# Kernel tuning notes

Hardware: AMD Instinct MI355X
Metric: run time of the kernel (lower is better)

## Reference

```python
import jax, jax.numpy as jnp
import numpy as np

INPUT_LAYER_SIZE = 40960 * 2
LAYER1_SIZE = 512
LAYER2_SIZE = 32
LAYER3_SIZE = 32
BATCH = 4096


def setup_inputs() -> dict:
    key = jax.random.key(0)
    ks = jax.random.split(key, 10)
    # Sparse one-hot style features: mostly zeros with ~30 active entries per side.
    def sparse_features(k, n_active=30):
        kidx, = jax.random.split(k, 1)
        idx = jax.random.randint(kidx, (BATCH, n_active), 0, 40960)
        feats = jnp.zeros((BATCH, 40960), dtype=jnp.float32)
        return feats.at[jnp.arange(BATCH)[:, None], idx].set(1.0)
    w_features = sparse_features(ks[0])
    b_features = sparse_features(ks[1])
    s_in = 1.0 / np.sqrt(INPUT_LAYER_SIZE)
    s1 = 1.0 / np.sqrt(LAYER1_SIZE)
    s2 = 1.0 / np.sqrt(LAYER2_SIZE)
    s3 = 1.0 / np.sqrt(LAYER3_SIZE)
    return {
        "w_features": w_features,
        "b_features": b_features,
        "W_in": jax.random.uniform(ks[2], (LAYER1_SIZE, INPUT_LAYER_SIZE), jnp.float32, -s_in, s_in),
        "b_in": jax.random.uniform(ks[3], (LAYER1_SIZE,), jnp.float32, -s_in, s_in),
        "W1": jax.random.uniform(ks[4], (LAYER2_SIZE, LAYER1_SIZE), jnp.float32, -s1, s1),
        "b1": jax.random.uniform(ks[5], (LAYER2_SIZE,), jnp.float32, -s1, s1),
        "W2": jax.random.uniform(ks[6], (LAYER3_SIZE, LAYER2_SIZE), jnp.float32, -s2, s2),
        "b2": jax.random.uniform(ks[7], (LAYER3_SIZE,), jnp.float32, -s2, s2),
        "W3": jax.random.uniform(ks[8], (1, LAYER3_SIZE), jnp.float32, -s3, s3),
        "b3": jax.random.uniform(ks[9], (1,), jnp.float32, -s3, s3),
    }


def reference(w_features, b_features, W_in, b_in, W1, b1, W2, b2, W3, b3):
    # Concatenate both perspectives: [B, 81920]
    x = jnp.concatenate([w_features, b_features], axis=1)
    # Huge sparse-input accumulator layer (the kernel-headroom op)
    accum = x @ W_in.T + b_in                       # [B, 512]
    l1 = jnp.clip(accum, 0.0, 1.0)                  # clipped ReLU
    l2 = jnp.clip(l1 @ W1.T + b1, 0.0, 1.0)         # [B, 32]
    l3 = jnp.clip(l2 @ W2.T + b2, 0.0, 1.0)         # [B, 32]
    return l3 @ W3.T + b3                           # [B, 1]
```

## Files before the change

kernel.cpp:

```cpp
#include <hip/hip_runtime.h>
#include <hip/hip_bf16.h>

#define IN_PER_SIDE   40960
#define IN_TOTAL      81920
#define L1            512
#define L2            32
#define L3_           32
#define BATCH         4096
#define MAXIDX        128

typedef float        v4f __attribute__((ext_vector_type(4)));
typedef float        v8f __attribute__((ext_vector_type(8)));
typedef _Float16     v4h __attribute__((ext_vector_type(4)));
typedef _Float16     v8h __attribute__((ext_vector_type(8)));
typedef unsigned int v4u __attribute__((ext_vector_type(4)));

#define WT_BYTES ((size_t)IN_TOTAL * L1 * sizeof(_Float16))

__global__ __launch_bounds__(256) void transpose_win(
    const float* __restrict__ W, _Float16* __restrict__ WTh)
{
    __shared__ float tile[64][65];
    const int jt = blockIdx.x * 64;
    const int ot = blockIdx.y * 64;

    {
        const int tx = threadIdx.x & 15;
        const int ty = threadIdx.x >> 4;
#pragma unroll
        for (int k = 0; k < 4; ++k) {
            const int o = ty + 16 * k;
            const v4f* p = (const v4f*)&W[(size_t)(ot + o) * IN_TOTAL + jt + 4 * tx];
            v4f v = __builtin_nontemporal_load(p);
            tile[4 * tx + 0][o] = v.x;
            tile[4 * tx + 1][o] = v.y;
            tile[4 * tx + 2][o] = v.z;
            tile[4 * tx + 3][o] = v.w;
        }
    }
    __syncthreads();
    {
        const int tx = threadIdx.x & 7;
        const int ty = threadIdx.x >> 3;
#pragma unroll
        for (int k = 0; k < 2; ++k) {
            const int j = ty + 32 * k;
            v8f v;
#pragma unroll
            for (int c = 0; c < 8; ++c) v[c] = tile[j][8 * tx + c];
            v8h h = __builtin_convertvector(v, v8h);
            *(v8h*)&WTh[(size_t)(jt + j) * L1 + ot + 8 * tx] = h;
        }
    }
}

__global__ __launch_bounds__(512) void nnue_fused(
    const float* __restrict__ wf, const float* __restrict__ bfeat,
    const _Float16* __restrict__ WTh,
    const float* __restrict__ b_in,
    const float* __restrict__ W1, const float* __restrict__ b1,
    const float* __restrict__ W2, const float* __restrict__ b2,
    const float* __restrict__ W3, const float* __restrict__ b3,
    float* __restrict__ out)
{
    const int b = blockIdx.x;
    const int t = threadIdx.x;

    __shared__ int   sidx[MAXIDX];
    __shared__ int   scnt;
    __shared__ float accs[8 * 64 * 9];
    __shared__ float l1s[L1];
    __shared__ float l2acc[L2];
    __shared__ float l2s[L2];
    __shared__ float l3s[L3_];

    if (t == 0) { scnt = 0; sidx[0] = 0; }
    __syncthreads();

    const v4u* wrow = (const v4u*)(wf    + (size_t)b * IN_PER_SIDE);
    const v4u* brow = (const v4u*)(bfeat + (size_t)b * IN_PER_SIDE);

    for (int g = 0; g < 5; ++g) {
        v4u a0, a1, a2, a3, c0, c1, c2, c3;
        {
            const int i0 = t + (4 * g + 0) * 512;
            const int i1 = t + (4 * g + 1) * 512;
            const int i2 = t + (4 * g + 2) * 512;
            const int i3 = t + (4 * g + 3) * 512;
            a0 = wrow[i0]; a1 = wrow[i1]; a2 = wrow[i2]; a3 = wrow[i3];
            c0 = brow[i0]; c1 = brow[i1]; c2 = brow[i2]; c3 = brow[i3];
        }
#pragma unroll
        for (int u = 0; u < 4; ++u) {
            const v4u a = (u == 0) ? a0 : (u == 1) ? a1 : (u == 2) ? a2 : a3;
            const v4u c = (u == 0) ? c0 : (u == 1) ? c1 : (u == 2) ? c2 : c3;
            const int i = t + (4 * g + u) * 512;
            if (a.x | a.y | a.z | a.w) {
                if (a.x) sidx[atomicAdd(&scnt, 1)] = 4 * i + 0;
                if (a.y) sidx[atomicAdd(&scnt, 1)] = 4 * i + 1;
                if (a.z) sidx[atomicAdd(&scnt, 1)] = 4 * i + 2;
                if (a.w) sidx[atomicAdd(&scnt, 1)] = 4 * i + 3;
            }
            if (c.x | c.y | c.z | c.w) {
                if (c.x) sidx[atomicAdd(&scnt, 1)] = IN_PER_SIDE + 4 * i + 0;
                if (c.y) sidx[atomicAdd(&scnt, 1)] = IN_PER_SIDE + 4 * i + 1;
                if (c.z) sidx[atomicAdd(&scnt, 1)] = IN_PER_SIDE + 4 * i + 2;
                if (c.w) sidx[atomicAdd(&scnt, 1)] = IN_PER_SIDE + 4 * i + 3;
            }
        }
    }
    __syncthreads();

    const int n = scnt;
    const int w = t >> 6;
    const int l = t & 63;
    const v8h* WTH8 = (const v8h*)WTh;

    v8f acc0 = {0, 0, 0, 0, 0, 0, 0, 0};
    v8f acc1 = {0, 0, 0, 0, 0, 0, 0, 0};
    const int J     = (n + 7) >> 3;
    const int Jeven = (J + 1) & ~1;

    {
        const int f0 = w, f1 = w + 8;
        v8h h0 = WTH8[(size_t)sidx[f0 < n ? f0 : 0] * 64 + l];
        float s0 = (f0 < n) ? 1.0f : 0.0f;
        v8h h1 = WTH8[(size_t)sidx[f1 < n ? f1 : 0] * 64 + l];
        float s1 = (f1 < n) ? 1.0f : 0.0f;
        for (int j = 2; j < Jeven; j += 2) {
            const int g0 = w + 8 * j, g1 = g0 + 8;
            v8h p0 = WTH8[(size_t)sidx[g0 < n ? g0 : 0] * 64 + l];
            const float u0 = (g0 < n) ? 1.0f : 0.0f;
            v8h p1 = WTH8[(size_t)sidx[g1 < n ? g1 : 0] * 64 + l];
            const float u1 = (g1 < n) ? 1.0f : 0.0f;
            acc0 += s0 * __builtin_convertvector(h0, v8f);
            acc1 += s1 * __builtin_convertvector(h1, v8f);
            h0 = p0; s0 = u0; h1 = p1; s1 = u1;
        }
        acc0 += s0 * __builtin_convertvector(h0, v8f);
        acc1 += s1 * __builtin_convertvector(h1, v8f);
    }
    acc0 += acc1;

    {
        float* dst = &accs[(w * 64 + l) * 9];
#pragma unroll
        for (int i = 0; i < 8; ++i) dst[i] = acc0[i];
    }
    __syncthreads();

    {
        const int ll = t >> 3, c = t & 7;
        float s = 0.0f;
#pragma unroll
        for (int ww = 0; ww < 8; ++ww) s += accs[(ww * 64 + ll) * 9 + c];
        l1s[t] = fminf(fmaxf(s + b_in[t], 0.0f), 1.0f);
    }
    __syncthreads();

    {
        const int kk = t >> 4;
        const int gg = t & 15;
        const float* wp = W1 + (size_t)kk * L1;
        float p = 0.0f;
        for (int o = gg; o < L1; o += 16) p += wp[o] * l1s[o];
#pragma unroll
        for (int off = 8; off > 0; off >>= 1) p += __shfl_down(p, off, 16);
        if (gg == 0) l2acc[kk] = p;
    }
    __syncthreads();
    if (t < L2) l2s[t] = fminf(fmaxf(l2acc[t] + b1[t], 0.0f), 1.0f);
    __syncthreads();

    if (t < L3_) {
        const float* wp = W2 + (size_t)t * L2;
        float p = b2[t];
#pragma unroll
        for (int q = 0; q < L2; ++q) p += wp[q] * l2s[q];
        l3s[t] = fminf(fmaxf(p, 0.0f), 1.0f);
    }
    __syncthreads();

    if (t == 0) {
        float p = b3[0];
#pragma unroll
        for (int q = 0; q < L3_; ++q) p += W3[q] * l3s[q];
        out[b] = p;
    }
}

__global__ __launch_bounds__(512) void nnue_fallback(
    const float* __restrict__ wf, const float* __restrict__ bfeat,
    const float* __restrict__ W_in, const float* __restrict__ b_in,
    const float* __restrict__ W1, const float* __restrict__ b1,
    const float* __restrict__ W2, const float* __restrict__ b2,
    const float* __restrict__ W3, const float* __restrict__ b3,
    float* __restrict__ out)
{
    const int b = blockIdx.x;
    const int t = threadIdx.x;
    __shared__ int   idxs[MAXIDX];
    __shared__ int   scnt;
    __shared__ float l1s[L1];
    __shared__ float l2acc[L2];
    __shared__ float l2s[L2];
    __shared__ float l3s[L3_];

    if (t == 0) scnt = 0;
    __syncthreads();
    const v4f* wrow = (const v4f*)(wf    + (size_t)b * IN_PER_SIDE);
    const v4f* brow = (const v4f*)(bfeat + (size_t)b * IN_PER_SIDE);
    for (int i = t; i < IN_PER_SIDE / 4; i += 512) {
        v4f v = wrow[i];
        if (v.x != 0.0f) idxs[atomicAdd(&scnt, 1)] = 4 * i + 0;
        if (v.y != 0.0f) idxs[atomicAdd(&scnt, 1)] = 4 * i + 1;
        if (v.z != 0.0f) idxs[atomicAdd(&scnt, 1)] = 4 * i + 2;
        if (v.w != 0.0f) idxs[atomicAdd(&scnt, 1)] = 4 * i + 3;
        v4f u = brow[i];
        if (u.x != 0.0f) idxs[atomicAdd(&scnt, 1)] = IN_PER_SIDE + 4 * i + 0;
        if (u.y != 0.0f) idxs[atomicAdd(&scnt, 1)] = IN_PER_SIDE + 4 * i + 1;
        if (u.z != 0.0f) idxs[atomicAdd(&scnt, 1)] = IN_PER_SIDE + 4 * i + 2;
        if (u.w != 0.0f) idxs[atomicAdd(&scnt, 1)] = IN_PER_SIDE + 4 * i + 3;
    }
    __syncthreads();
    const int n = scnt;
    float a0 = 0.0f;
    const float* row = W_in + (size_t)t * IN_TOTAL;
    for (int i = 0; i < n; ++i) a0 += row[idxs[i]];
    l1s[t] = fminf(fmaxf(b_in[t] + a0, 0.0f), 1.0f);
    __syncthreads();
    {
        const int k = t >> 4, g = t & 15;
        const float* wp = W1 + (size_t)k * L1;
        float p = 0.0f;
        for (int o = g; o < L1; o += 16) p += wp[o] * l1s[o];
#pragma unroll
        for (int off = 8; off > 0; off >>= 1) p += __shfl_down(p, off, 16);
        if (g == 0) l2acc[k] = p;
    }
    __syncthreads();
    if (t < L2) l2s[t] = fminf(fmaxf(l2acc[t] + b1[t], 0.0f), 1.0f);
    __syncthreads();
    if (t < L3_) {
        const float* wp = W2 + (size_t)t * L2;
        float p = b2[t];
#pragma unroll
        for (int q = 0; q < L2; ++q) p += wp[q] * l2s[q];
        l3s[t] = fminf(fmaxf(p, 0.0f), 1.0f);
    }
    __syncthreads();
    if (t == 0) {
        float p = b3[0];
#pragma unroll
        for (int q = 0; q < L3_; ++q) p += W3[q] * l3s[q];
        out[b] = p;
    }
}

extern "C" void kernel_launch(void* const* d_in, const int* in_sizes, int n_in,
                              void* d_out, int out_size, void* d_ws, size_t ws_size,
                              hipStream_t stream) {
    const float* wf   = (const float*)d_in[0];
    const float* bfeat= (const float*)d_in[1];
    const float* W_in = (const float*)d_in[2];
    const float* b_in = (const float*)d_in[3];
    const float* W1   = (const float*)d_in[4];
    const float* b1   = (const float*)d_in[5];
    const float* W2   = (const float*)d_in[6];
    const float* b2   = (const float*)d_in[7];
    const float* W3   = (const float*)d_in[8];
    const float* b3   = (const float*)d_in[9];
    float* out = (float*)d_out;

    if (ws_size >= WT_BYTES) {
        _Float16* WTh = (_Float16*)d_ws;
        dim3 grid(IN_TOTAL / 64, L1 / 64);
        transpose_win<<<grid, 256, 0, stream>>>(W_in, WTh);
        nnue_fused<<<BATCH, 512, 0, stream>>>(
            wf, bfeat, WTh, b_in, W1, b1, W2, b2, W3, b3, out);
    } else {
        nnue_fallback<<<BATCH, 512, 0, stream>>>(
            wf, bfeat, W_in, b_in, W1, b1, W2, b2, W3, b3, out);
    }
}
```

Before: 1.359 ms.

## Fuse weight transpose and sparse index scan into one cooperative persistent kernel

Adds a persistent cooperative kernel that transposes and converts W_in to fp16 while the same blocks scan the feature rows into a global index list. A grid-wide sync then separates this from the gather/accumulate and MLP stage. The goal is to overlap the feature scan with the weight transpose and to remove a separate launch. The cost is a grid sync, an extra global round trip for the indices, and a cap of 1024 persistent blocks that may reduce parallelism in the gather stage. It falls back to the old two-kernel path if the cooperative launch is unavailable.

After: 1.542 ms. 1.13x slower.

```diff
diff --git a/kernel.cpp b/kernel.cpp
--- a/kernel.cpp
+++ b/kernel.cpp
@@ -1,5 +1,8 @@
 #include <hip/hip_runtime.h>
 #include <hip/hip_bf16.h>
+#include <hip/hip_cooperative_groups.h>
+
+namespace cg = cooperative_groups;
 
 #define IN_PER_SIDE   40960
 #define IN_TOTAL      81920
@@ -16,6 +19,179 @@
 typedef unsigned int v4u __attribute__((ext_vector_type(4)));
 
 #define WT_BYTES ((size_t)IN_TOTAL * L1 * sizeof(_Float16))
+#define CNT_OFF  WT_BYTES
+#define IDX_OFF  (WT_BYTES + 16384)
+#define WS_NEED  (IDX_OFF + (size_t)BATCH * MAXIDX * 4)
+
+__global__ __launch_bounds__(512) void nnue_mega(
+    const float* __restrict__ W, _Float16* __restrict__ WTh,
+    const float* __restrict__ wf, const float* __restrict__ bfeat,
+    int* __restrict__ cnt, int* __restrict__ idxg,
+    const float* __restrict__ b_in,
+    const float* __restrict__ W1, const float* __restrict__ b1,
+    const float* __restrict__ W2, const float* __restrict__ b2,
+    const float* __restrict__ W3, const float* __restrict__ b3,
+    float* __restrict__ out)
+{
+    const int t = threadIdx.x;
+    const int G = gridDim.x;
+
+    __shared__ __align__(16) char smem[8 * 64 * 9 * 4];
+    float (*tile)[65] = reinterpret_cast<float (*)[65]>(smem);
+    float* accs = reinterpret_cast<float*>(smem);
+    __shared__ int   sidx[MAXIDX];
+    __shared__ int   scnt;
+    __shared__ float l1s[L1];
+    __shared__ float l2acc[L2];
+    __shared__ float l2s[L2];
+    __shared__ float l3s[L3_];
+
+    for (int tid = blockIdx.x; tid < 1280 * 8; tid += G) {
+        const int jt = (tid % 1280) * 64;
+        const int ot = (tid / 1280) * 64;
+        {
+            const int tx = t & 15;
+            const int ty = t >> 4;
+#pragma unroll
+            for (int k = 0; k < 2; ++k) {
+                const int o = ty + 32 * k;
+                const v4f* p = (const v4f*)&W[(size_t)(ot + o) * IN_TOTAL + jt + 4 * tx];
+                v4f v = __builtin_nontemporal_load(p);
+                tile[4 * tx + 0][o] = v.x;
+                tile[4 * tx + 1][o] = v.y;
+                tile[4 * tx + 2][o] = v.z;
+                tile[4 * tx + 3][o] = v.w;
+            }
+        }
+        __syncthreads();
+        {
+            const int tx = t & 7;
+            const int ty = t >> 3;
+            v8f v;
+#pragma unroll
+            for (int c = 0; c < 8; ++c) v[c] = tile[ty][8 * tx + c];
+            v8h h = __builtin_convertvector(v, v8h);
+            *(v8h*)&WTh[(size_t)(jt + ty) * L1 + ot + 8 * tx] = h;
+        }
+        __syncthreads();
+    }
+
+    for (int row = blockIdx.x; row < BATCH; row += G) {
+        if (t == 0) scnt = 0;
+        __syncthreads();
+        const v4u* wrow = (const v4u*)(wf    + (size_t)row * IN_PER_SIDE);
+        const v4u* brow = (const v4u*)(bfeat + (size_t)row * IN_PER_SIDE);
+        for (int i = t; i < IN_PER_SIDE / 4; i += 512) {
+            v4u a = __builtin_nontemporal_load(wrow + i);
+            v4u c = __builtin_nontemporal_load(brow + i);
+            if (a.x | a.y | a.z | a.w) {
+                if (a.x) { int p = atomicAdd(&scnt, 1); if (p < MAXIDX) sidx[p] = 4 * i + 0; }
+                if (a.y) { int p = atomicAdd(&scnt, 1); if (p < MAXIDX) sidx[p] = 4 * i + 1; }
+                if (a.z) { int p = atomicAdd(&scnt, 1); if (p < MAXIDX) sidx[p] = 4 * i + 2; }
+                if (a.w) { int p = atomicAdd(&scnt, 1); if (p < MAXIDX) sidx[p] = 4 * i + 3; }
+            }
+            if (c.x | c.y | c.z | c.w) {
+                if (c.x) { int p = atomicAdd(&scnt, 1); if (p < MAXIDX) sidx[p] = IN_PER_SIDE + 4 * i + 0; }
+                if (c.y) { int p = atomicAdd(&scnt, 1); if (p < MAXIDX) sidx[p] = IN_PER_SIDE + 4 * i + 1; }
+                if (c.z) { int p = atomicAdd(&scnt, 1); if (p < MAXIDX) sidx[p] = IN_PER_SIDE + 4 * i + 2; }
+                if (c.w) { int p = atomicAdd(&scnt, 1); if (p < MAXIDX) sidx[p] = IN_PER_SIDE + 4 * i + 3; }
+            }
+        }
+        __syncthreads();
+        const int nn = min(scnt, MAXIDX);
+        if (t < nn) idxg[(size_t)row * MAXIDX + t] = sidx[t];
+        if (t == 0) cnt[row] = nn;
+        __syncthreads();
+    }
+
+    __threadfence();
+    cg::this_grid().sync();
+
+    const int w = t >> 6;
+    const int l = t & 63;
+    const v8h* WTH8 = (const v8h*)WTh;
+
+    for (int row = blockIdx.x; row < BATCH; row += G) {
+        const int n = cnt[row];
+        if (t < MAXIDX) {
+            const int g = idxg[(size_t)row * MAXIDX + t];
+            sidx[t] = (t < n) ? g : 0;
+        }
+        __syncthreads();
+
+        v8f acc0 = {0, 0, 0, 0, 0, 0, 0, 0};
+        v8f acc1 = {0, 0, 0, 0, 0, 0, 0, 0};
+        const int J     = (n + 7) >> 3;
+        const int Jeven = (J + 1) & ~1;
+        {
+            const int f0 = w, f1 = w + 8;
+            v8h h0 = WTH8[(size_t)sidx[f0 < n ? f0 : 0] * 64 + l];
+            float s0 = (f0 < n) ? 1.0f : 0.0f;
+            v8h h1 = WTH8[(size_t)sidx[f1 < n ? f1 : 0] * 64 + l];
+            float s1 = (f1 < n) ? 1.0f : 0.0f;
+            for (int j = 2; j < Jeven; j += 2) {
+                const int g0 = w + 8 * j, g1 = g0 + 8;
+                v8h p0 = WTH8[(size_t)sidx[g0 < n ? g0 : 0] * 64 + l];
+                const float u0 = (g0 < n) ? 1.0f : 0.0f;
+                v8h p1 = WTH8[(size_t)sidx[g1 < n ? g1 : 0] * 64 + l];
+                const float u1 = (g1 < n) ? 1.0f : 0.0f;
+                acc0 += s0 * __builtin_convertvector(h0, v8f);
+                acc1 += s1 * __builtin_convertvector(h1, v8f);
+                h0 = p0; s0 = u0; h1 = p1; s1 = u1;
+            }
+            acc0 += s0 * __builtin_convertvector(h0, v8f);
+            acc1 += s1 * __builtin_convertvector(h1, v8f);
+        }
+        acc0 += acc1;
+
+        {
+            float* dst = &accs[(w * 64 + l) * 9];
+#pragma unroll
+            for (int i = 0; i < 8; ++i) dst[i] = acc0[i];
+        }
+        __syncthreads();
+
+        {
+            const int ll = t >> 3, c = t & 7;
+            float s = 0.0f;
+#pragma unroll
+            for (int ww = 0; ww < 8; ++ww) s += accs[(ww * 64 + ll) * 9 + c];
+            l1s[t] = fminf(fmaxf(s + b_in[t], 0.0f), 1.0f);
+        }
+        __syncthreads();
+
+        {
+            const int kk = t >> 4;
+            const int gg = t & 15;
+            const float* wp = W1 + (size_t)kk * L1;
+            float p = 0.0f;
+            for (int o = gg; o < L1; o += 16) p += wp[o] * l1s[o];
+#pragma unroll
+            for (int off = 8; off > 0; off >>= 1) p += __shfl_down(p, off, 16);
+            if (gg == 0) l2acc[kk] = p;
+        }
+        __syncthreads();
+        if (t < L2) l2s[t] = fminf(fmaxf(l2acc[t] + b1[t], 0.0f), 1.0f);
+        __syncthreads();
+
+        if (t < L3_) {
+            const float* wp = W2 + (size_t)t * L2;
+            float p = b2[t];
+#pragma unroll
+            for (int q = 0; q < L2; ++q) p += wp[q] * l2s[q];
+            l3s[t] = fminf(fmaxf(p, 0.0f), 1.0f);
+        }
+        __syncthreads();
+
+        if (t == 0) {
+            float p = b3[0];
+#pragma unroll
+            for (int q = 0; q < L3_; ++q) p += W3[q] * l3s[q];
+            out[row] = p;
+        }
+        __syncthreads();
+    }
+}
 
 __global__ __launch_bounds__(256) void transpose_win(
     const float* __restrict__ W, _Float16* __restrict__ WTh)
@@ -23,7 +199,6 @@
     __shared__ float tile[64][65];
     const int jt = blockIdx.x * 64;
     const int ot = blockIdx.y * 64;
-
     {
         const int tx = threadIdx.x & 15;
         const int ty = threadIdx.x >> 4;
@@ -79,34 +254,20 @@
 
     const v4u* wrow = (const v4u*)(wf    + (size_t)b * IN_PER_SIDE);
     const v4u* brow = (const v4u*)(bfeat + (size_t)b * IN_PER_SIDE);
-
-    for (int g = 0; g < 5; ++g) {
-        v4u a0, a1, a2, a3, c0, c1, c2, c3;
-        {
-            const int i0 = t + (4 * g + 0) * 512;
-            const int i1 = t + (4 * g + 1) * 512;
-            const int i2 = t + (4 * g + 2) * 512;
-            const int i3 = t + (4 * g + 3) * 512;
-            a0 = wrow[i0]; a1 = wrow[i1]; a2 = wrow[i2]; a3 = wrow[i3];
-            c0 = brow[i0]; c1 = brow[i1]; c2 = brow[i2]; c3 = brow[i3];
-        }
-#pragma unroll
-        for (int u = 0; u < 4; ++u) {
-            const v4u a = (u == 0) ? a0 : (u == 1) ? a1 : (u == 2) ? a2 : a3;
-            const v4u c = (u == 0) ? c0 : (u == 1) ? c1 : (u == 2) ? c2 : c3;
-            const int i = t + (4 * g + u) * 512;
-            if (a.x | a.y | a.z | a.w) {
-                if (a.x) sidx[atomicAdd(&scnt, 1)] = 4 * i + 0;
-                if (a.y) sidx[atomicAdd(&scnt, 1)] = 4 * i + 1;
-                if (a.z) sidx[atomicAdd(&scnt, 1)] = 4 * i + 2;
-                if (a.w) sidx[atomicAdd(&scnt, 1)] = 4 * i + 3;
-            }
-            if (c.x | c.y | c.z | c.w) {
-                if (c.x) sidx[atomicAdd(&scnt, 1)] = IN_PER_SIDE + 4 * i + 0;
-                if (c.y) sidx[atomicAdd(&scnt, 1)] = IN_PER_SIDE + 4 * i + 1;
-                if (c.z) sidx[atomicAdd(&scnt, 1)] = IN_PER_SIDE + 4 * i + 2;
-                if (c.w) sidx[atomicAdd(&scnt, 1)] = IN_PER_SIDE + 4 * i + 3;
-            }
+    for (int i = t; i < IN_PER_SIDE / 4; i += 512) {
+        v4u a = __builtin_nontemporal_load(wrow + i);
+        v4u c = __builtin_nontemporal_load(brow + i);
+        if (a.x | a.y | a.z | a.w) {
+            if (a.x) sidx[atomicAdd(&scnt, 1)] = 4 * i + 0;
+            if (a.y) sidx[atomicAdd(&scnt, 1)] = 4 * i + 1;
+            if (a.z) sidx[atomicAdd(&scnt, 1)] = 4 * i + 2;
+            if (a.w) sidx[atomicAdd(&scnt, 1)] = 4 * i + 3;
+        }
+        if (c.x | c.y | c.z | c.w) {
+            if (c.x) sidx[atomicAdd(&scnt, 1)] = IN_PER_SIDE + 4 * i + 0;
+            if (c.y) sidx[atomicAdd(&scnt, 1)] = IN_PER_SIDE + 4 * i + 1;
+            if (c.z) sidx[atomicAdd(&scnt, 1)] = IN_PER_SIDE + 4 * i + 2;
+            if (c.w) sidx[atomicAdd(&scnt, 1)] = IN_PER_SIDE + 4 * i + 3;
         }
     }
     __syncthreads();
@@ -120,7 +281,6 @@
     v8f acc1 = {0, 0, 0, 0, 0, 0, 0, 0};
     const int J     = (n + 7) >> 3;
     const int Jeven = (J + 1) & ~1;
-
     {
         const int f0 = w, f1 = w + 8;
         v8h h0 = WTH8[(size_t)sidx[f0 < n ? f0 : 0] * 64 + l];
@@ -157,7 +317,6 @@
         l1s[t] = fminf(fmaxf(s + b_in[t], 0.0f), 1.0f);
     }
     __syncthreads();
-
     {
         const int kk = t >> 4;
         const int gg = t & 15;
@@ -171,7 +330,6 @@
     __syncthreads();
     if (t < L2) l2s[t] = fminf(fmaxf(l2acc[t] + b1[t], 0.0f), 1.0f);
     __syncthreads();
-
     if (t < L3_) {
         const float* wp = W2 + (size_t)t * L2;
         float p = b2[t];
@@ -180,7 +338,6 @@
         l3s[t] = fminf(fmaxf(p, 0.0f), 1.0f);
     }
     __syncthreads();
-
     if (t == 0) {
         float p = b3[0];
 #pragma unroll
@@ -272,14 +429,60 @@
     const float* b3   = (const float*)d_in[9];
     float* out = (float*)d_out;
 
-    if (ws_size >= WT_BYTES) {
-        _Float16* WTh = (_Float16*)d_ws;
-        dim3 grid(IN_TOTAL / 64, L1 / 64);
-        transpose_win<<<grid, 256, 0, stream>>>(W_in, WTh);
-        nnue_fused<<<BATCH, 512, 0, stream>>>(
-            wf, bfeat, WTh, b_in, W1, b1, W2, b2, W3, b3, out);
-    } else {
-        nnue_fallback<<<BATCH, 512, 0, stream>>>(
-            wf, bfeat, W_in, b_in, W1, b1, W2, b2, W3, b3, out);
+    static int g_grid = -2;
+    if (g_grid == -2) {
+        int dev = 0;
+        hipDeviceProp_t prop{};
+        int nb = 0;
+        if (hipGetDevice(&dev) == hipSuccess &&
+            hipGetDeviceProperties(&prop, dev) == hipSuccess &&
+            prop.cooperativeLaunch &&
+            hipOccupancyMaxActiveBlocksPerMultiprocessor(&nb, nnue_mega, 512, 0) == hipSuccess &&
+            nb >= 1) {
+            long cap = (long)nb * prop.multiProcessorCount;
+            g_grid = (int)(cap < 1024 ? cap : 1024);
+        } else {
+            g_grid = -1;
+        }
+    }
+
+    bool launched = false;
+    if (ws_size >= WS_NEED && g_grid > 0) {
+        char* ws = (char*)d_ws;
+        _Float16* WTh = (_Float16*)ws;
+        int* cnt  = (int*)(ws + CNT_OFF);
+        int* idxg = (int*)(ws + IDX_OFF);
+
+        const float* W_a = W_in;  _Float16* WTh_a = WTh;
+        const float* wf_a = wf;   const float* bf_a = bfeat;
+        int* cnt_a = cnt;         int* idxg_a = idxg;
+        const float* bin_a = b_in;
+        const float* W1_a = W1;   const float* b1_a = b1;
+        const float* W2_a = W2;   const float* b2_a = b2;
+        const float* W3_a = W3;   const float* b3_a = b3;
+        float* out_a = out;
+        void* args[] = {&W_a, &WTh_a, &wf_a, &bf_a, &cnt_a, &idxg_a,
+                        &bin_a, &W1_a, &b1_a, &W2_a, &b2_a, &W3_a, &b3_a, &out_a};
+        hipError_t e = hipLaunchCooperativeKernel(
+            nnue_mega, dim3(g_grid), dim3(512), args, 0, stream);
+        if (e == hipSuccess) {
+            launched = true;
+        } else {
+            (void)hipGetLastError();
+            g_grid = -1;
+        }
+    }
+
+    if (!launched) {
+        if (ws_size >= WT_BYTES) {
+            _Float16* WTh = (_Float16*)d_ws;
+            dim3 grid(IN_TOTAL / 64, L1 / 64);
+            transpose_win<<<grid, 256, 0, stream>>>(W_in, WTh);
+            nnue_fused<<<BATCH, 512, 0, stream>>>(
+                wf, bfeat, WTh, b_in, W1, b1, W2, b2, W3, b3, out);
+        } else {
+            nnue_fallback<<<BATCH, 512, 0, stream>>>(
+                wf, bfeat, W_in, b_in, W1, b1, W2, b2, W3, b3, out);
+        }
     }
 }
```
